# Kernel optimization log

Measured on AMD Instinct MI355X. Metric: run time of the kernel, lower is better.

## Reference

```python
import jax, jax.numpy as jnp
import numpy as np

B = 8192          # number of bags/users
L = 50            # items per bag (uniform)
NNZ = B * L
VOCAB = 100000
D = 64            # embedding_dim
ATT = 64          # att_dim
K = 4             # acc_user_num


def setup_inputs() -> dict:
    key = jax.random.key(0)
    k1, k2, k3, k4, k5 = jax.random.split(key, 5)
    # flat CSR indices, sorted within each row (module assumes coalesced order)
    idx = jax.random.randint(k1, (B, L), 0, VOCAB, dtype=jnp.int64)
    input_ = jnp.sort(idx, axis=1).reshape(NNZ)
    offsets = (jnp.arange(B, dtype=jnp.int64) * L)
    emb_weight = jax.random.normal(k2, (VOCAB, D), dtype=jnp.float32) * 0.05
    proj_w = jax.random.normal(k3, (ATT, D), dtype=jnp.float32) * (1.0 / np.sqrt(D))
    proj_b = jax.random.normal(k4, (ATT,), dtype=jnp.float32) * 0.01
    att_h = jax.random.truncated_normal(k5, -2.0, 2.0, (ATT, K), dtype=jnp.float32) * 0.01
    return {"input_": input_, "offsets": offsets, "emb_weight": emb_weight,
            "proj_w": proj_w, "proj_b": proj_b, "att_h": att_h}


def reference(input_, offsets, emb_weight, proj_w, proj_b, att_h):
    nnz = input_.shape[0]
    nseg = offsets.shape[0]
    # segment id for each flat element (offsets are sorted row starts)
    seg = jnp.searchsorted(offsets, jnp.arange(nnz), side="right") - 1  # [nnz]
    att_emb = emb_weight[input_]                                        # [nnz, D]
    att = jnp.tanh(att_emb @ proj_w.T + proj_b) @ att_h                 # [nnz, K]
    # ragged per-segment softmax over each attention column
    m = jax.ops.segment_max(att, seg, num_segments=nseg)                # [B, K]
    e = jnp.exp(att - m[seg])
    s = jax.ops.segment_sum(e, seg, num_segments=nseg)                  # [B, K]
    smax = e / s[seg]                                                   # [nnz, K]
    # weighted segment-sum pooling -> [B, K, D]
    weighted = smax[:, :, None] * att_emb[:, None, :]                   # [nnz, K, D]
    result = jax.ops.segment_sum(weighted, seg, num_segments=nseg)
    return result
```

## Files before the change

### kernel.cpp

```cpp
#include <hip/hip_runtime.h>
#include <hip/hip_bf16.h>

typedef __attribute__((ext_vector_type(4))) float  f32x4;
typedef __attribute__((ext_vector_type(4))) short  s16x4;
typedef __attribute__((ext_vector_type(8))) short  s16x8;

#define SH 72

__device__ inline short f2bf(float x) {
    return __builtin_bit_cast(short, __float2bfloat16(x));
}
__device__ inline float bf2f(short s) {
    return __builtin_bit_cast(float, ((int)(unsigned short)s) << 16);
}
__device__ inline s16x8 pack8(f32x4 a, f32x4 b) {
    s16x8 r;
    r[0] = f2bf(a[0]); r[1] = f2bf(a[1]); r[2] = f2bf(a[2]); r[3] = f2bf(a[3]);
    r[4] = f2bf(b[0]); r[5] = f2bf(b[1]); r[6] = f2bf(b[2]); r[7] = f2bf(b[3]);
    return r;
}

__global__ __launch_bounds__(256) void conv_kernel(
    const float* __restrict__ emb, short* __restrict__ emb_bf, int n8)
{
    int t = blockIdx.x * 256 + threadIdx.x;
    int stride = gridDim.x * 256;
    for (int i = t; i < n8; i += stride) {
        f32x4 a = *(const f32x4*)(emb + (size_t)i * 8);
        f32x4 b = *(const f32x4*)(emb + (size_t)i * 8 + 4);
        *(s16x8*)(emb_bf + (size_t)i * 8) = pack8(a, b);
    }
}

__global__ __launch_bounds__(256, 4) void pooled_attn_kernel(
    const int*   __restrict__ input_,
    const int*   __restrict__ offsets,
    const short* __restrict__ emb_bf,
    const float* __restrict__ pw,
    const float* __restrict__ pb,
    const float* __restrict__ ah,
    float*       __restrict__ out,
    int B, int nnz)
{
    __shared__ __align__(16) short s_pw [64 * SH];
    __shared__ __align__(16) short s_ahp[2 * 64 * 8];
    __shared__ __align__(16) float s_bias[64];
    __shared__ __align__(16) short s_h_all[4][16 * SH];
    __shared__ __align__(16) float s_w_all[4][64 * 4];

    const int tid  = threadIdx.x;
    const int lane = tid & 63;
    const int wv   = tid >> 6;
    const int col  = lane & 15;
    const int quad = lane >> 4;
    short* sh = s_h_all[wv];
    float* sw = s_w_all[wv];

    {
        int r = tid >> 2, seg = tid & 3;
        const float* rp = pw + r * 64 + seg * 16;
        f32x4 a0 = *(const f32x4*)(rp);
        f32x4 a1 = *(const f32x4*)(rp + 4);
        f32x4 a2 = *(const f32x4*)(rp + 8);
        f32x4 a3 = *(const f32x4*)(rp + 12);
        *(s16x8*)(s_pw + r * SH + seg * 16)     = pack8(a0, a1);
        *(s16x8*)(s_pw + r * SH + seg * 16 + 8) = pack8(a2, a3);
    }
    if (tid < 128) {
        int c = tid >> 6, l = tid & 63;
        int q = l >> 4, cc = l & 15;
        s16x8 v;
        #pragma unroll
        for (int j = 0; j < 8; ++j) {
            int a = c * 32 + q * 8 + j;
            v[j] = (cc < 4) ? f2bf(ah[a * 4 + cc]) : (short)0;
        }
        *(s16x8*)(s_ahp + (c * 64 + l) * 8) = v;
    }
    if (tid < 64) s_bias[tid] = pb[tid];
    __syncthreads();

    const s16x8 ahA0 = *(const s16x8*)(s_ahp + lane * 8);
    const s16x8 ahA1 = *(const s16x8*)(s_ahp + (64 + lane) * 8);
    s16x8 pwA[4][2];
    #pragma unroll
    for (int mt = 0; mt < 4; ++mt) {
        pwA[mt][0] = *(const s16x8*)(s_pw + (mt * 16 + col) * SH + quad * 8);
        pwA[mt][1] = *(const s16x8*)(s_pw + (mt * 16 + col) * SH + 32 + quad * 8);
    }

    const int bag = blockIdx.x * 4 + wv;
    if (bag >= B) return;
    const int start = offsets[bag];
    const int end   = (bag + 1 < B) ? offsets[bag + 1] : nnz;
    int n = end - start;
    if (n > 64) n = 64;
    if (n < 1) {
        float* op = out + (size_t)bag * 256 + lane;
        op[0] = 0.f; op[64] = 0.f; op[128] = 0.f; op[192] = 0.f;
        return;
    }
    const int idx_l = input_[start + (lane < n ? lane : n - 1)];

    f32x4 attv[4];
    #pragma unroll
    for (int nt = 0; nt < 4; ++nt) {
        int row = __shfl(idx_l, nt * 16 + col);
        const short* rp = emb_bf + (size_t)(unsigned)row * 64 + quad * 8;
        s16x8 eB0 = *(const s16x8*)(rp);
        s16x8 eB1 = *(const s16x8*)(rp + 32);

        #pragma unroll
        for (int mt = 0; mt < 4; ++mt) {
            f32x4 acc = *(const f32x4*)(s_bias + mt * 16 + quad * 4);
            acc = __builtin_amdgcn_mfma_f32_16x16x32_bf16(pwA[mt][0], eB0, acc, 0, 0, 0);
            acc = __builtin_amdgcn_mfma_f32_16x16x32_bf16(pwA[mt][1], eB1, acc, 0, 0, 0);
            s16x4 hp;
            #pragma unroll
            for (int r = 0; r < 4; ++r) {
                float z = acc[r];
                float t2 = z * z;
                float h = z * (1.f + t2 * (-0.33333334f +
                               t2 * (0.13333333f + t2 * (-0.05396825f))));
                hp[r] = f2bf(h);
            }
            *(s16x4*)(sh + col * SH + mt * 16 + quad * 4) = hp;
        }
        f32x4 a2 = {0.f, 0.f, 0.f, 0.f};
        s16x8 b20 = *(const s16x8*)(sh + col * SH + quad * 8);
        s16x8 b21 = *(const s16x8*)(sh + col * SH + 32 + quad * 8);
        a2 = __builtin_amdgcn_mfma_f32_16x16x32_bf16(ahA0, b20, a2, 0, 0, 0);
        a2 = __builtin_amdgcn_mfma_f32_16x16x32_bf16(ahA1, b21, a2, 0, 0, 0);
        attv[nt] = a2;
    }

    f32x4 ssum = {0.f, 0.f, 0.f, 0.f};
    #pragma unroll
    for (int nt = 0; nt < 4; ++nt) {
        const bool pad = (nt * 16 + col >= n);
        #pragma unroll
        for (int k = 0; k < 4; ++k) {
            float e = __expf(attv[nt][k]);
            e = pad ? 0.f : e;
            attv[nt][k] = e;
            ssum[k] += e;
        }
    }
    if (quad == 0) {
        #pragma unroll
        for (int t = 0; t < 4; ++t)
            *(f32x4*)(sw + (t * 16 + col) * 4) = attv[t];
    }

    float eb0[16], eb1[16];
    #pragma unroll
    for (int c = 0; c < 16; ++c) {
        int row = __builtin_amdgcn_readlane(idx_l, c);
        eb0[c] = bf2f(emb_bf[(size_t)(unsigned)row * 64 + lane]);
    }
    #pragma unroll
    for (int c = 0; c < 16; ++c) {
        int row = __builtin_amdgcn_readlane(idx_l, 16 + c);
        eb1[c] = bf2f(emb_bf[(size_t)(unsigned)row * 64 + lane]);
    }

    #pragma unroll
    for (int m = 1; m <= 8; m <<= 1)
        #pragma unroll
        for (int k = 0; k < 4; ++k)
            ssum[k] += __shfl_xor(ssum[k], m, 64);
    f32x4 rs;
    #pragma unroll
    for (int k = 0; k < 4; ++k)
        rs[k] = __builtin_amdgcn_rcpf(ssum[k]);

    f32x4 po = {0.f, 0.f, 0.f, 0.f};
    #pragma unroll
    for (int t = 0; t < 4; ++t) {
        float* ebc = (t & 1) ? eb1 : eb0;
        #pragma unroll
        for (int c = 0; c < 16; ++c) {
            f32x4 w = *(const f32x4*)(sw + (t * 16 + c) * 4);
            float ev = ebc[c];
            po[0] = fmaf(w[0], ev, po[0]);
            po[1] = fmaf(w[1], ev, po[1]);
            po[2] = fmaf(w[2], ev, po[2]);
            po[3] = fmaf(w[3], ev, po[3]);
        }
        if (t < 2) {
            #pragma unroll
            for (int c = 0; c < 16; ++c) {
                int row = __builtin_amdgcn_readlane(idx_l, (t + 2) * 16 + c);
                ebc[c] = bf2f(emb_bf[(size_t)(unsigned)row * 64 + lane]);
            }
        }
    }
    float* op = out + (size_t)bag * 256 + lane;
    op[0]   = po[0] * rs[0];
    op[64]  = po[1] * rs[1];
    op[128] = po[2] * rs[2];
    op[192] = po[3] * rs[3];
}

extern "C" void kernel_launch(void* const* d_in, const int* in_sizes, int n_in,
                              void* d_out, int out_size, void* d_ws, size_t ws_size,
                              hipStream_t stream) {
    const int*   input_  = (const int*)d_in[0];
    const int*   offsets = (const int*)d_in[1];
    const float* emb     = (const float*)d_in[2];
    const float* pw      = (const float*)d_in[3];
    const float* pb      = (const float*)d_in[4];
    const float* ah      = (const float*)d_in[5];
    float* out = (float*)d_out;
    const int nnz   = in_sizes[0];
    const int B     = in_sizes[1];
    const int vocab_elems = in_sizes[2];

    short* emb_bf = (short*)d_ws;

    conv_kernel<<<1024, 256, 0, stream>>>(emb, emb_bf, vocab_elems / 8);
    pooled_attn_kernel<<<(B + 3) / 4, 256, 0, stream>>>(input_, offsets, emb_bf,
                                                        pw, pb, ah, out, B, nnz);
}
```

Measured before the change: 108.5 us.

## Fuse softmax-weighted pooling into the per-tile loop to cut register pressure

```diff
diff --git a/kernel.cpp b/kernel.cpp
--- a/kernel.cpp
+++ b/kernel.cpp
@@ -43,18 +43,17 @@
     int B, int nnz)
 {
     __shared__ __align__(16) short s_pw [64 * SH];
-    __shared__ __align__(16) short s_ahp[2 * 64 * 8];
     __shared__ __align__(16) float s_bias[64];
     __shared__ __align__(16) short s_h_all[4][16 * SH];
-    __shared__ __align__(16) float s_w_all[4][64 * 4];
+    __shared__ __align__(16) float s_w_all[4][16 * 4];
 
     const int tid  = threadIdx.x;
     const int lane = tid & 63;
     const int wv   = tid >> 6;
     const int col  = lane & 15;
     const int quad = lane >> 4;
-    short* sh = s_h_all[wv];
-    float* sw = s_w_all[wv];
+    short* sh  = s_h_all[wv];
+    float* swt = s_w_all[wv];
 
     {
         int r = tid >> 2, seg = tid & 3;
@@ -66,27 +65,19 @@
         *(s16x8*)(s_pw + r * SH + seg * 16)     = pack8(a0, a1);
         *(s16x8*)(s_pw + r * SH + seg * 16 + 8) = pack8(a2, a3);
     }
-    if (tid < 128) {
-        int c = tid >> 6, l = tid & 63;
-        int q = l >> 4, cc = l & 15;
-        s16x8 v;
-        #pragma unroll
-        for (int j = 0; j < 8; ++j) {
-            int a = c * 32 + q * 8 + j;
-            v[j] = (cc < 4) ? f2bf(ah[a * 4 + cc]) : (short)0;
-        }
-        *(s16x8*)(s_ahp + (c * 64 + l) * 8) = v;
-    }
     if (tid < 64) s_bias[tid] = pb[tid];
     __syncthreads();
 
-    const s16x8 ahA0 = *(const s16x8*)(s_ahp + lane * 8);
-    const s16x8 ahA1 = *(const s16x8*)(s_ahp + (64 + lane) * 8);
-    s16x8 pwA[4][2];
-    #pragma unroll
-    for (int mt = 0; mt < 4; ++mt) {
-        pwA[mt][0] = *(const s16x8*)(s_pw + (mt * 16 + col) * SH + quad * 8);
-        pwA[mt][1] = *(const s16x8*)(s_pw + (mt * 16 + col) * SH + 32 + quad * 8);
+    s16x8 ahA0, ahA1;
+    {
+        s16x8 v0, v1;
+        #pragma unroll
+        for (int j = 0; j < 8; ++j) {
+            int a0 = quad * 8 + j, a1 = 32 + quad * 8 + j;
+            v0[j] = (col < 4) ? f2bf(ah[a0 * 4 + col]) : (short)0;
+            v1[j] = (col < 4) ? f2bf(ah[a1 * 4 + col]) : (short)0;
+        }
+        ahA0 = v0; ahA1 = v1;
     }
 
     const int bag = blockIdx.x * 4 + wv;
@@ -102,19 +93,25 @@
     }
     const int idx_l = input_[start + (lane < n ? lane : n - 1)];
 
-    f32x4 attv[4];
+    f32x4 po[4];
     #pragma unroll
+    for (int k = 0; k < 4; ++k) po[k] = f32x4{0.f, 0.f, 0.f, 0.f};
+    f32x4 ssum = {0.f, 0.f, 0.f, 0.f};
+
+    #pragma unroll 1
     for (int nt = 0; nt < 4; ++nt) {
-        int row = __shfl(idx_l, nt * 16 + col);
-        const short* rp = emb_bf + (size_t)(unsigned)row * 64 + quad * 8;
+        int rowf = __shfl(idx_l, nt * 16 + col);
+        const short* rp = emb_bf + (size_t)(unsigned)rowf * 64 + quad * 8;
         s16x8 eB0 = *(const s16x8*)(rp);
         s16x8 eB1 = *(const s16x8*)(rp + 32);
 
         #pragma unroll
         for (int mt = 0; mt < 4; ++mt) {
+            s16x8 w0 = *(const s16x8*)(s_pw + (mt * 16 + col) * SH + quad * 8);
+            s16x8 w1 = *(const s16x8*)(s_pw + (mt * 16 + col) * SH + 32 + quad * 8);
             f32x4 acc = *(const f32x4*)(s_bias + mt * 16 + quad * 4);
-            acc = __builtin_amdgcn_mfma_f32_16x16x32_bf16(pwA[mt][0], eB0, acc, 0, 0, 0);
-            acc = __builtin_amdgcn_mfma_f32_16x16x32_bf16(pwA[mt][1], eB1, acc, 0, 0, 0);
+            acc = __builtin_amdgcn_mfma_f32_16x16x32_bf16(w0, eB0, acc, 0, 0, 0);
+            acc = __builtin_amdgcn_mfma_f32_16x16x32_bf16(w1, eB1, acc, 0, 0, 0);
             s16x4 hp;
             #pragma unroll
             for (int r = 0; r < 4; ++r) {
@@ -126,80 +123,69 @@
             }
             *(s16x4*)(sh + col * SH + mt * 16 + quad * 4) = hp;
         }
-        f32x4 a2 = {0.f, 0.f, 0.f, 0.f};
+        f32x4 av = {0.f, 0.f, 0.f, 0.f};
         s16x8 b20 = *(const s16x8*)(sh + col * SH + quad * 8);
         s16x8 b21 = *(const s16x8*)(sh + col * SH + 32 + quad * 8);
-        a2 = __builtin_amdgcn_mfma_f32_16x16x32_bf16(ahA0, b20, a2, 0, 0, 0);
-        a2 = __builtin_amdgcn_mfma_f32_16x16x32_bf16(ahA1, b21, a2, 0, 0, 0);
-        attv[nt] = a2;
-    }
-
-    f32x4 ssum = {0.f, 0.f, 0.f, 0.f};
+        av = __builtin_amdgcn_mfma_f32_16x16x32_bf16(ahA0, b20, av, 0, 0, 0);
+        av = __builtin_amdgcn_mfma_f32_16x16x32_bf16(ahA1, b21, av, 0, 0, 0);
+
+        if (quad == 0) {
+            const bool pad = (nt * 16 + col >= n);
+            f32x4 ev;
+            #pragma unroll
+            for (int k = 0; k < 4; ++k) {
+                float e = __expf(av[k]);
+                ev[k] = pad ? 0.f : e;
+            }
+            ssum += ev;
+            *(f32x4*)(swt + col * 4) = ev;
+        }
+
+        #pragma unroll
+        for (int g = 0; g < 4; ++g) {
+            int it = nt * 16 + quad * 4 + g;
+            int prow = __shfl(idx_l, it);
+            s16x4 e4 = *(const s16x4*)(emb_bf + (size_t)(unsigned)prow * 64 + col * 4);
+            f32x4 w = *(const f32x4*)(swt + (quad * 4 + g) * 4);
+            f32x4 ef;
+            ef[0] = bf2f(e4[0]); ef[1] = bf2f(e4[1]);
+            ef[2] = bf2f(e4[2]); ef[3] = bf2f(e4[3]);
+            #pragma unroll
+            for (int k = 0; k < 4; ++k) {
+                po[k][0] = fmaf(w[k], ef[0], po[k][0]);
+                po[k][1] = fmaf(w[k], ef[1], po[k][1]);
+                po[k][2] = fmaf(w[k], ef[2], po[k][2]);
+                po[k][3] = fmaf(w[k], ef[3], po[k][3]);
+            }
+        }
+    }
+
     #pragma unroll
-    for (int nt = 0; nt < 4; ++nt) {
-        const bool pad = (nt * 16 + col >= n);
+    for (int m = 16; m <= 32; m <<= 1)
         #pragma unroll
         for (int k = 0; k < 4; ++k) {
-            float e = __expf(attv[nt][k]);
-            e = pad ? 0.f : e;
-            attv[nt][k] = e;
-            ssum[k] += e;
-        }
-    }
+            po[k][0] += __shfl_xor(po[k][0], m, 64);
+            po[k][1] += __shfl_xor(po[k][1], m, 64);
+            po[k][2] += __shfl_xor(po[k][2], m, 64);
+            po[k][3] += __shfl_xor(po[k][3], m, 64);
+        }
+
     if (quad == 0) {
         #pragma unroll
-        for (int t = 0; t < 4; ++t)
-            *(f32x4*)(sw + (t * 16 + col) * 4) = attv[t];
-    }
-
-    float eb0[16], eb1[16];
-    #pragma unroll
-    for (int c = 0; c < 16; ++c) {
-        int row = __builtin_amdgcn_readlane(idx_l, c);
-        eb0[c] = bf2f(emb_bf[(size_t)(unsigned)row * 64 + lane]);
-    }
-    #pragma unroll
-    for (int c = 0; c < 16; ++c) {
-        int row = __builtin_amdgcn_readlane(idx_l, 16 + c);
-        eb1[c] = bf2f(emb_bf[(size_t)(unsigned)row * 64 + lane]);
-    }
-
-    #pragma unroll
-    for (int m = 1; m <= 8; m <<= 1)
-        #pragma unroll
-        for (int k = 0; k < 4; ++k)
-            ssum[k] += __shfl_xor(ssum[k], m, 64);
-    f32x4 rs;
-    #pragma unroll
-    for (int k = 0; k < 4; ++k)
-        rs[k] = __builtin_amdgcn_rcpf(ssum[k]);
-
-    f32x4 po = {0.f, 0.f, 0.f, 0.f};
-    #pragma unroll
-    for (int t = 0; t < 4; ++t) {
-        float* ebc = (t & 1) ? eb1 : eb0;
-        #pragma unroll
-        for (int c = 0; c < 16; ++c) {
-            f32x4 w = *(const f32x4*)(sw + (t * 16 + c) * 4);
-            float ev = ebc[c];
-            po[0] = fmaf(w[0], ev, po[0]);
-            po[1] = fmaf(w[1], ev, po[1]);
-            po[2] = fmaf(w[2], ev, po[2]);
-            po[3] = fmaf(w[3], ev, po[3]);
-        }
-        if (t < 2) {
-            #pragma unroll
-            for (int c = 0; c < 16; ++c) {
-                int row = __builtin_amdgcn_readlane(idx_l, (t + 2) * 16 + c);
-                ebc[c] = bf2f(emb_bf[(size_t)(unsigned)row * 64 + lane]);
-            }
-        }
-    }
-    float* op = out + (size_t)bag * 256 + lane;
-    op[0]   = po[0] * rs[0];
-    op[64]  = po[1] * rs[1];
-    op[128] = po[2] * rs[2];
-    op[192] = po[3] * rs[3];
+        for (int m = 1; m <= 8; m <<= 1)
+            #pragma unroll
+            for (int k = 0; k < 4; ++k)
+                ssum[k] += __shfl_xor(ssum[k], m, 64);
+        float* op = out + (size_t)bag * 256 + col * 4;
+        #pragma unroll
+        for (int k = 0; k < 4; ++k) {
+            float rs = __builtin_amdgcn_rcpf(ssum[k]);
+            f32x4 o;
+            o[0] = po[k][0] * rs; o[1] = po[k][1] * rs;
+            o[2] = po[k][2] * rs; o[3] = po[k][3] * rs;
+            *(f32x4*)(op + k * 64) = o;
+        }
+    }
 }
 
 extern "C" void kernel_launch(void* const* d_in, const int* in_sizes, int n_in,
```

Result: slower. 111.8 us (+3.0%).

## Precompute per-vocab attention logits in prep kernel, simplify pooling to table lookup

Applied to the files above, without the earlier changes.

```diff
diff --git a/kernel.cpp b/kernel.cpp
--- a/kernel.cpp
+++ b/kernel.cpp
@@ -4,8 +4,6 @@
 typedef __attribute__((ext_vector_type(4))) float  f32x4;
 typedef __attribute__((ext_vector_type(4))) short  s16x4;
 typedef __attribute__((ext_vector_type(8))) short  s16x8;
-
-#define SH 72
 
 __device__ inline short f2bf(float x) {
     return __builtin_bit_cast(short, __float2bfloat16(x));
@@ -20,74 +18,93 @@
     return r;
 }
 
-__global__ __launch_bounds__(256) void conv_kernel(
-    const float* __restrict__ emb, short* __restrict__ emb_bf, int n8)
+__global__ __launch_bounds__(256, 4) void prep_kernel(
+    const float* __restrict__ emb,
+    const float* __restrict__ pw,
+    const float* __restrict__ pb,
+    const float* __restrict__ ah,
+    short*       __restrict__ emb_bf,
+    float*       __restrict__ att_tab,
+    int vocab)
 {
-    int t = blockIdx.x * 256 + threadIdx.x;
-    int stride = gridDim.x * 256;
-    for (int i = t; i < n8; i += stride) {
-        f32x4 a = *(const f32x4*)(emb + (size_t)i * 8);
-        f32x4 b = *(const f32x4*)(emb + (size_t)i * 8 + 4);
-        *(s16x8*)(emb_bf + (size_t)i * 8) = pack8(a, b);
+    const int lane = threadIdx.x & 63;
+    const int wv   = threadIdx.x >> 6;
+    const int col  = lane & 15;
+    const int quad = lane >> 4;
+
+    const int w = blockIdx.x * 4 + wv;
+    const int base = w * 16;
+    if (base >= vocab) return;
+    const int v = base + col;
+    const int vc = (v < vocab) ? v : vocab - 1;
+
+    s16x8 pwA[4][2];
+    #pragma unroll
+    for (int mt = 0; mt < 4; ++mt) {
+        const float* rp = pw + (mt * 16 + col) * 64 + quad * 8;
+        #pragma unroll
+        for (int c = 0; c < 2; ++c) {
+            f32x4 u0 = *(const f32x4*)(rp + c * 32);
+            f32x4 u1 = *(const f32x4*)(rp + c * 32 + 4);
+            pwA[mt][c] = pack8(u0, u1);
+        }
     }
+
+    const float* rp = emb + (size_t)vc * 64 + quad * 8;
+    f32x4 e00 = *(const f32x4*)(rp);
+    f32x4 e01 = *(const f32x4*)(rp + 4);
+    f32x4 e10 = *(const f32x4*)(rp + 32);
+    f32x4 e11 = *(const f32x4*)(rp + 36);
+    s16x8 eB0 = pack8(e00, e01);
+    s16x8 eB1 = pack8(e10, e11);
+
+    if (v < vocab) {
+        *(s16x8*)(emb_bf + (size_t)v * 64 + quad * 8)      = eB0;
+        *(s16x8*)(emb_bf + (size_t)v * 64 + 32 + quad * 8) = eB1;
+    }
+
+    f32x4 p = {0.f, 0.f, 0.f, 0.f};
+    #pragma unroll
+    for (int mt = 0; mt < 4; ++mt) {
+        f32x4 acc = *(const f32x4*)(pb + mt * 16 + quad * 4);
+        acc = __builtin_amdgcn_mfma_f32_16x16x32_bf16(pwA[mt][0], eB0, acc, 0, 0, 0);
+        acc = __builtin_amdgcn_mfma_f32_16x16x32_bf16(pwA[mt][1], eB1, acc, 0, 0, 0);
+        #pragma unroll
+        for (int r = 0; r < 4; ++r) {
+            float z = acc[r];
+            float t2 = z * z;
+            float h = z * (1.f + t2 * (-0.33333334f +
+                           t2 * (0.13333333f + t2 * (-0.05396825f))));
+            f32x4 ahv = *(const f32x4*)(ah + (mt * 16 + quad * 4 + r) * 4);
+            p[0] = fmaf(h, ahv[0], p[0]);
+            p[1] = fmaf(h, ahv[1], p[1]);
+            p[2] = fmaf(h, ahv[2], p[2]);
+            p[3] = fmaf(h, ahv[3], p[3]);
+        }
+    }
+    #pragma unroll
+    for (int m = 16; m <= 32; m <<= 1)
+        #pragma unroll
+        for (int k = 0; k < 4; ++k)
+            p[k] += __shfl_xor(p[k], m, 64);
+
+    if (quad == 0 && v < vocab)
+        *(f32x4*)(att_tab + (size_t)v * 4) = p;
 }
 
-__global__ __launch_bounds__(256, 4) void pooled_attn_kernel(
+__global__ __launch_bounds__(256, 4) void pool_kernel(
     const int*   __restrict__ input_,
     const int*   __restrict__ offsets,
     const short* __restrict__ emb_bf,
-    const float* __restrict__ pw,
-    const float* __restrict__ pb,
-    const float* __restrict__ ah,
+    const float* __restrict__ att_tab,
     float*       __restrict__ out,
     int B, int nnz)
 {
-    __shared__ __align__(16) short s_pw [64 * SH];
-    __shared__ __align__(16) short s_ahp[2 * 64 * 8];
-    __shared__ __align__(16) float s_bias[64];
-    __shared__ __align__(16) short s_h_all[4][16 * SH];
     __shared__ __align__(16) float s_w_all[4][64 * 4];
 
-    const int tid  = threadIdx.x;
-    const int lane = tid & 63;
-    const int wv   = tid >> 6;
-    const int col  = lane & 15;
-    const int quad = lane >> 4;
-    short* sh = s_h_all[wv];
+    const int lane = threadIdx.x & 63;
+    const int wv   = threadIdx.x >> 6;
     float* sw = s_w_all[wv];
-
-    {
-        int r = tid >> 2, seg = tid & 3;
-        const float* rp = pw + r * 64 + seg * 16;
-        f32x4 a0 = *(const f32x4*)(rp);
-        f32x4 a1 = *(const f32x4*)(rp + 4);
-        f32x4 a2 = *(const f32x4*)(rp + 8);
-        f32x4 a3 = *(const f32x4*)(rp + 12);
-        *(s16x8*)(s_pw + r * SH + seg * 16)     = pack8(a0, a1);
-        *(s16x8*)(s_pw + r * SH + seg * 16 + 8) = pack8(a2, a3);
-    }
-    if (tid < 128) {
-        int c = tid >> 6, l = tid & 63;
-        int q = l >> 4, cc = l & 15;
-        s16x8 v;
-        #pragma unroll
-        for (int j = 0; j < 8; ++j) {
-            int a = c * 32 + q * 8 + j;
-            v[j] = (cc < 4) ? f2bf(ah[a * 4 + cc]) : (short)0;
-        }
-        *(s16x8*)(s_ahp + (c * 64 + l) * 8) = v;
-    }
-    if (tid < 64) s_bias[tid] = pb[tid];
-    __syncthreads();
-
-    const s16x8 ahA0 = *(const s16x8*)(s_ahp + lane * 8);
-    const s16x8 ahA1 = *(const s16x8*)(s_ahp + (64 + lane) * 8);
-    s16x8 pwA[4][2];
-    #pragma unroll
-    for (int mt = 0; mt < 4; ++mt) {
-        pwA[mt][0] = *(const s16x8*)(s_pw + (mt * 16 + col) * SH + quad * 8);
-        pwA[mt][1] = *(const s16x8*)(s_pw + (mt * 16 + col) * SH + 32 + quad * 8);
-    }
 
     const int bag = blockIdx.x * 4 + wv;
     if (bag >= B) return;
@@ -102,70 +119,23 @@
     }
     const int idx_l = input_[start + (lane < n ? lane : n - 1)];
 
-    f32x4 attv[4];
+    f32x4 av = *(const f32x4*)(att_tab + (size_t)(unsigned)idx_l * 4);
+    f32x4 e;
     #pragma unroll
-    for (int nt = 0; nt < 4; ++nt) {
-        int row = __shfl(idx_l, nt * 16 + col);
-        const short* rp = emb_bf + (size_t)(unsigned)row * 64 + quad * 8;
-        s16x8 eB0 = *(const s16x8*)(rp);
-        s16x8 eB1 = *(const s16x8*)(rp + 32);
+    for (int k = 0; k < 4; ++k)
+        e[k] = (lane < n) ? __expf(av[k]) : 0.f;
+    *(f32x4*)(sw + lane * 4) = e;
 
-        #pragma unroll
-        for (int mt = 0; mt < 4; ++mt) {
-            f32x4 acc = *(const f32x4*)(s_bias + mt * 16 + quad * 4);
-            acc = __builtin_amdgcn_mfma_f32_16x16x32_bf16(pwA[mt][0], eB0, acc, 0, 0, 0);
-            acc = __builtin_amdgcn_mfma_f32_16x16x32_bf16(pwA[mt][1], eB1, acc, 0, 0, 0);
-            s16x4 hp;
-            #pragma unroll
-            for (int r = 0; r < 4; ++r) {
-                float z = acc[r];
-                float t2 = z * z;
-                float h = z * (1.f + t2 * (-0.33333334f +
-                               t2 * (0.13333333f + t2 * (-0.05396825f))));
-                hp[r] = f2bf(h);
-            }
-            *(s16x4*)(sh + col * SH + mt * 16 + quad * 4) = hp;
-        }
-        f32x4 a2 = {0.f, 0.f, 0.f, 0.f};
-        s16x8 b20 = *(const s16x8*)(sh + col * SH + quad * 8);
-        s16x8 b21 = *(const s16x8*)(sh + col * SH + 32 + quad * 8);
-        a2 = __builtin_amdgcn_mfma_f32_16x16x32_bf16(ahA0, b20, a2, 0, 0, 0);
-        a2 = __builtin_amdgcn_mfma_f32_16x16x32_bf16(ahA1, b21, a2, 0, 0, 0);
-        attv[nt] = a2;
+    float eb[2][8];
+    #pragma unroll
+    for (int c = 0; c < 8; ++c) {
+        int row = __builtin_amdgcn_readlane(idx_l, c);
+        eb[0][c] = bf2f(emb_bf[(size_t)(unsigned)row * 64 + lane]);
     }
 
-    f32x4 ssum = {0.f, 0.f, 0.f, 0.f};
+    f32x4 ssum = e;
     #pragma unroll
-    for (int nt = 0; nt < 4; ++nt) {
-        const bool pad = (nt * 16 + col >= n);
-        #pragma unroll
-        for (int k = 0; k < 4; ++k) {
-            float e = __expf(attv[nt][k]);
-            e = pad ? 0.f : e;
-            attv[nt][k] = e;
-            ssum[k] += e;
-        }
-    }
-    if (quad == 0) {
-        #pragma unroll
-        for (int t = 0; t < 4; ++t)
-            *(f32x4*)(sw + (t * 16 + col) * 4) = attv[t];
-    }
-
-    float eb0[16], eb1[16];
-    #pragma unroll
-    for (int c = 0; c < 16; ++c) {
-        int row = __builtin_amdgcn_readlane(idx_l, c);
-        eb0[c] = bf2f(emb_bf[(size_t)(unsigned)row * 64 + lane]);
-    }
-    #pragma unroll
-    for (int c = 0; c < 16; ++c) {
-        int row = __builtin_amdgcn_readlane(idx_l, 16 + c);
-        eb1[c] = bf2f(emb_bf[(size_t)(unsigned)row * 64 + lane]);
-    }
-
-    #pragma unroll
-    for (int m = 1; m <= 8; m <<= 1)
+    for (int m = 1; m <= 32; m <<= 1)
         #pragma unroll
         for (int k = 0; k < 4; ++k)
             ssum[k] += __shfl_xor(ssum[k], m, 64);
@@ -176,23 +146,22 @@
 
     f32x4 po = {0.f, 0.f, 0.f, 0.f};
     #pragma unroll
-    for (int t = 0; t < 4; ++t) {
-        float* ebc = (t & 1) ? eb1 : eb0;
+    for (int g = 0; g < 8; ++g) {
+        if (g < 7) {
+            #pragma unroll
+            for (int c = 0; c < 8; ++c) {
+                int row = __builtin_amdgcn_readlane(idx_l, (g + 1) * 8 + c);
+                eb[(g + 1) & 1][c] = bf2f(emb_bf[(size_t)(unsigned)row * 64 + lane]);
+            }
+        }
         #pragma unroll
-        for (int c = 0; c < 16; ++c) {
-            f32x4 w = *(const f32x4*)(sw + (t * 16 + c) * 4);
-            float ev = ebc[c];
+        for (int c = 0; c < 8; ++c) {
+            f32x4 w = *(const f32x4*)(sw + (g * 8 + c) * 4);
+            float ev = eb[g & 1][c];
             po[0] = fmaf(w[0], ev, po[0]);
             po[1] = fmaf(w[1], ev, po[1]);
             po[2] = fmaf(w[2], ev, po[2]);
             po[3] = fmaf(w[3], ev, po[3]);
-        }
-        if (t < 2) {
-            #pragma unroll
-            for (int c = 0; c < 16; ++c) {
-                int row = __builtin_amdgcn_readlane(idx_l, (t + 2) * 16 + c);
-                ebc[c] = bf2f(emb_bf[(size_t)(unsigned)row * 64 + lane]);
-            }
         }
     }
     float* op = out + (size_t)bag * 256 + lane;
@@ -214,11 +183,14 @@
     float* out = (float*)d_out;
     const int nnz   = in_sizes[0];
     const int B     = in_sizes[1];
-    const int vocab_elems = in_sizes[2];
+    const int vocab = in_sizes[2] / 64;
 
-    short* emb_bf = (short*)d_ws;
+    float* att_tab = (float*)d_ws;
+    short* emb_bf  = (short*)((char*)d_ws + (16 << 20));
 
-    conv_kernel<<<1024, 256, 0, stream>>>(emb, emb_bf, vocab_elems / 8);
-    pooled_attn_kernel<<<(B + 3) / 4, 256, 0, stream>>>(input_, offsets, emb_bf,
-                                                        pw, pb, ah, out, B, nnz);
+    const int groups = (vocab + 15) / 16;
+    prep_kernel<<<(groups + 3) / 4, 256, 0, stream>>>(emb, pw, pb, ah,
+                                                      emb_bf, att_tab, vocab);
+    pool_kernel<<<(B + 3) / 4, 256, 0, stream>>>(input_, offsets, emb_bf,
+                                                 att_tab, out, B, nnz);
 }
```

New measurement: 112.1 us. 1.03x slower.
